# Performance work log

Measured on AMD Instinct MI355X. Metric: run time of the kernel, lower is better.

## Reference

```python
import jax, jax.numpy as jnp
import numpy as np

B, T, C, H, E, MIN_E = 4, 2048, 1024, 128, 16, 2
IS_CAUSAL = False


def setup_inputs() -> dict:
    key = jax.random.key(0)
    ks = jax.random.split(key, 6)
    lim_qkv = float(np.sqrt(6.0 / (C + H)))
    inp = {
        "hidden_states": jax.random.normal(ks[0], (B, T, C), jnp.float32),
        "sim_matrix": jax.random.normal(ks[1], (C, E), jnp.float32),
        "gates": jnp.zeros((E,), jnp.float32),
        "q_proj": jax.random.uniform(ks[2], (E, C, H), jnp.float32, -lim_qkv, lim_qkv),
        "k_proj": jax.random.uniform(ks[3], (E, C, H), jnp.float32, -lim_qkv, lim_qkv),
        "v_proj": jax.random.uniform(ks[4], (E, C, H), jnp.float32, -lim_qkv, lim_qkv),
        "o_proj": jax.random.uniform(ks[5], (E, H, C), jnp.float32, -lim_qkv, lim_qkv),
    }
    return inp


def _forward(hidden_states, sim_matrix, gates, q_proj, k_proj, v_proj, o_proj):
    b, t, c = hidden_states.shape
    n = b * t
    x = hidden_states.reshape(n, c)

    # ---- gating (faithful to _gating_logic) ----
    xn = x / jnp.maximum(jnp.linalg.norm(x, axis=-1, keepdims=True), 1e-12)
    sn = sim_matrix / jnp.maximum(jnp.linalg.norm(sim_matrix, axis=0, keepdims=True), 1e-12)
    logits = xn @ sn - jax.nn.sigmoid(gates)          # [n, E]
    gated = jax.nn.relu(logits)
    # STE: forward = (gated > 0), backward = identity
    hard = (gated > 0).astype(gated.dtype)
    mask = gated + jax.lax.stop_gradient(hard - gated)
    inactive = (jnp.sum(hard, axis=1) == 0)
    # fallback: top-MIN_E logits for tokens with no active expert
    _, fb_idx = jax.lax.top_k(logits, MIN_E)
    fb = jnp.zeros((n, logits.shape[1]), gated.dtype).at[
        jnp.arange(n)[:, None], fb_idx].set(1.0)
    put = jax.lax.stop_gradient(inactive[:, None].astype(gated.dtype) * fb)
    mask = mask * (1.0 - put) + put                   # index_put semantics
    masked = jnp.where(mask > 0, gated, -jnp.inf)
    w = jax.nn.softmax(masked, axis=-1)               # routing weights [n, E]

    # ---- MoE dispatch/combine (dense-equivalent: w is exactly 0 where mask==0) ----
    def moe_proj(p):  # p: [E, C, H] -> [n, H]
        y = jnp.einsum('nc,ech->neh', x, p)
        return jnp.einsum('ne,neh->nh', w, y)

    q = moe_proj(q_proj).reshape(b, t, -1)
    k = moe_proj(k_proj).reshape(b, t, -1)
    v = moe_proj(v_proj).reshape(b, t, -1)

    # single-head SDPA, default scale 1/sqrt(head_dim)
    h = q.shape[-1]
    scores = jnp.einsum('bth,bsh->bts', q, k) / jnp.sqrt(jnp.asarray(h, q.dtype))
    if IS_CAUSAL and t > 1:
        causal = jnp.tril(jnp.ones((t, t), bool))
        scores = jnp.where(causal[None], scores, -jnp.inf)
    attn = jax.nn.softmax(scores, axis=-1)
    o = jnp.einsum('bts,bsh->bth', attn, v).reshape(n, h)

    # output MoE combine
    z = jnp.einsum('ne,nh->enh', w, o)                # [E, n, H]
    out = jnp.einsum('enh,ehc->nc', z, o_proj)
    return out.reshape(b, t, c)


def reference(hidden_states, sim_matrix, gates, q_proj, k_proj, v_proj, o_proj):
    return _forward(hidden_states, sim_matrix, gates, q_proj, k_proj, v_proj, o_proj)
```

## Files before the change

### kernel.cpp

```cpp
#include <hip/hip_runtime.h>
#include <hip/hip_bf16.h>
#include <math.h>

#define NBATCH 4
#define NT     2048
#define NC     1024
#define NH     128
#define NE     16
#define NTOK   (NBATCH * NT)
#define CAP    18432
#define NTILE_MAX 304

typedef __bf16 bf16x8 __attribute__((ext_vector_type(8)));
typedef __bf16 bf16x4 __attribute__((ext_vector_type(4)));
typedef float  f32x4  __attribute__((ext_vector_type(4)));

__device__ __forceinline__ __bf16 f2bf(float f) { return (__bf16)f; }

#define BARRIER() __builtin_amdgcn_s_barrier()
#define SFENCE()  __builtin_amdgcn_sched_barrier(0)
#define VMWAIT(n) asm volatile("s_waitcnt vmcnt(" #n ")" ::: "memory")
#define LGKMWAIT0() asm volatile("s_waitcnt lgkmcnt(0)" ::: "memory")

__device__ __forceinline__ void gl_lds16(const void* g, void* l) {
  __builtin_amdgcn_global_load_lds((const __attribute__((address_space(1))) void*)g,
                                   (__attribute__((address_space(3))) void*)l, 16, 0, 0);
}

__device__ __forceinline__ const __bf16* swz_src(const __bf16* row0, size_t stride,
                                                 int tid, int i) {
  int lin = (tid + 256 * i) * 16;
  int r = lin >> 7, cb = lin & 127;
  return row0 + (size_t)r * stride + ((cb ^ ((r & 7) << 4)) >> 1);
}

__global__ void k_prep(const float* __restrict__ sim, const float* __restrict__ gates,
                       double* __restrict__ snorm, double* __restrict__ sig) {
  int tid = threadIdx.x;
  int e = tid & 15, chunk = tid >> 4;
  double a = 0.0;
#pragma unroll 4
  for (int j = 0; j < 64; j++) {
    double v = (double)sim[(chunk * 64 + j) * NE + e];
    a += v * v;
  }
  __shared__ double red[16][17];
  red[chunk][e] = a;
  __syncthreads();
  if (tid < 16) {
    double s = 0.0;
    for (int k = 0; k < 16; k++) s += red[k][tid];
    snorm[tid] = fmax(sqrt(s), 1e-12);
    sig[tid] = 1.0 / (1.0 + exp(-(double)gates[tid]));
  }
}

__global__ __launch_bounds__(256, 1) void k_gating3(const float* __restrict__ x,
                                                    const float* __restrict__ sim,
                                                    const double* __restrict__ snorm,
                                                    const double* __restrict__ sig,
                                                    float* __restrict__ w_all,
                                                    int* __restrict__ counts,
                                                    __bf16* __restrict__ xbf) {
  __shared__ union {
    struct {
      float xs_[32][66];
      float ss_[16][66];
    } s;
    double red[8][32][4][17];
  } u;
  __shared__ float w_lds[32][16];
  __shared__ int cnt_lds[16];
  int tid = threadIdx.x;
  if (tid < 16) cnt_lds[tid] = 0;
  int cg = tid & 31, tkg = tid >> 5;
  int tok0 = blockIdx.x * 32;

  double acc[4][17];
#pragma unroll
  for (int t = 0; t < 4; t++)
#pragma unroll
    for (int i = 0; i < 17; i++) acc[t][i] = 0.0;

  int xr0 = tid >> 4, xc4 = (tid & 15) * 4;
  int sr = tid >> 2, se4 = (tid & 3) * 4;

  float4 xa, xb, sv;
  auto ldchunk = [&](int c0) {
    xa = *(const float4*)(x + (size_t)(tok0 + xr0) * NC + c0 + xc4);
    xb = *(const float4*)(x + (size_t)(tok0 + xr0 + 16) * NC + c0 + xc4);
    sv = *(const float4*)(sim + (size_t)(c0 + sr) * NE + se4);
  };
  auto stchunk = [&]() {
    *(float4*)&u.s.xs_[xr0][xc4] = xa;
    *(float4*)&u.s.xs_[xr0 + 16][xc4] = xb;
    u.s.ss_[se4 + 0][sr] = sv.x;
    u.s.ss_[se4 + 1][sr] = sv.y;
    u.s.ss_[se4 + 2][sr] = sv.z;
    u.s.ss_[se4 + 3][sr] = sv.w;
  };
  auto stxbf = [&](int c0) {
    bf16x4 a, b;
    a[0]=f2bf(xa.x); a[1]=f2bf(xa.y); a[2]=f2bf(xa.z); a[3]=f2bf(xa.w);
    b[0]=f2bf(xb.x); b[1]=f2bf(xb.y); b[2]=f2bf(xb.z); b[3]=f2bf(xb.w);
    *(bf16x4*)(xbf + (size_t)(tok0 + xr0) * NC + c0 + xc4) = a;
    *(bf16x4*)(xbf + (size_t)(tok0 + xr0 + 16) * NC + c0 + xc4) = b;
  };

  ldchunk(0);
  for (int ch = 0; ch < 16; ch++) {
    stchunk();
    stxbf(ch * 64);
    __syncthreads();
    if (ch < 15) ldchunk((ch + 1) * 64);
    double xd[4][2];
#pragma unroll
    for (int t = 0; t < 4; t++) {
      float2 xv = *(const float2*)&u.s.xs_[tkg * 4 + t][cg * 2];
      xd[t][0] = (double)xv.x;
      xd[t][1] = (double)xv.y;
      acc[t][16] += xd[t][0] * xd[t][0] + xd[t][1] * xd[t][1];
    }
#pragma unroll
    for (int e = 0; e < 16; e++) {
      float2 sv2 = *(const float2*)&u.s.ss_[e][cg * 2];
      double s0 = (double)sv2.x, s1 = (double)sv2.y;
#pragma unroll
      for (int t = 0; t < 4; t++)
        acc[t][e] += xd[t][0] * s0 + xd[t][1] * s1;
    }
    __syncthreads();
  }

#pragma unroll
  for (int t = 0; t < 4; t++)
#pragma unroll
    for (int i = 0; i < 17; i++)
      u.red[tkg][cg][t][i] = acc[t][i];
  __syncthreads();

  if (tid < 32) {
    double dots[17];
    for (int i = 0; i < 17; i++) {
      double s = 0.0;
      for (int c = 0; c < 32; c++) s += u.red[tid >> 2][c][tid & 3][i];
      dots[i] = s;
    }
    double xn = fmax(sqrt(dots[16]), 1e-12);
    double logits[NE];
    unsigned act = 0;
    int cnt = 0;
    for (int ee = 0; ee < NE; ee++) {
      logits[ee] = dots[ee] / (xn * snorm[ee]) - sig[ee];
      if (logits[ee] > 0.0) { act |= 1u << ee; cnt++; }
    }
    if (cnt == 0) {
      int i1 = 0; double b1 = logits[0];
      for (int ee = 1; ee < NE; ee++) if (logits[ee] > b1) { b1 = logits[ee]; i1 = ee; }
      int i2 = -1; double b2 = -1e300;
      for (int ee = 0; ee < NE; ee++) if (ee != i1 && logits[ee] > b2) { b2 = logits[ee]; i2 = ee; }
      act = (1u << i1) | (1u << i2);
    }
    double m = -1e300;
    for (int ee = 0; ee < NE; ee++) if ((act >> ee) & 1) m = fmax(m, fmax(logits[ee], 0.0));
    double s = 0.0, wvv[NE];
    for (int ee = 0; ee < NE; ee++) {
      if ((act >> ee) & 1) { wvv[ee] = exp(fmax(logits[ee], 0.0) - m); s += wvv[ee]; }
      else wvv[ee] = 0.0;
    }
    for (int ee = 0; ee < NE; ee++) {
      if ((act >> ee) & 1) {
        w_lds[tid][ee] = (float)(wvv[ee] / s);
        atomicAdd(&cnt_lds[ee], 1);
      } else w_lds[tid][ee] = 0.0f;
    }
  }
  __syncthreads();
  *(float2*)&w_all[(size_t)(tok0 + (tid >> 3)) * NE + (tid & 7) * 2] =
      *(const float2*)&w_lds[tid >> 3][(tid & 7) * 2];
  if (tid < 16 && cnt_lds[tid] > 0) atomicAdd(&counts[tid], cnt_lds[tid]);
}

__global__ void k_transpose_all(const float* __restrict__ qp, const float* __restrict__ kp,
                                const float* __restrict__ vp, const float* __restrict__ op,
                                __bf16* __restrict__ pqt, __bf16* __restrict__ pkt,
                                __bf16* __restrict__ pvt, __bf16* __restrict__ pot) {
  __shared__ float tile[32][33];
  int z = blockIdx.y;
  const float* in;
  __bf16* out;
  int R, Cd, g, r0, c0;
  if (z < 48) {
    int which = z >> 4; g = z & 15; R = 1024; Cd = 128;
    in = which == 0 ? qp : (which == 1 ? kp : vp);
    out = which == 0 ? pqt : (which == 1 ? pkt : pvt);
    r0 = (blockIdx.x >> 2) * 32; c0 = (blockIdx.x & 3) * 32;
  } else {
    g = z - 48; R = 128; Cd = 1024;
    in = op; out = pot;
    r0 = (blockIdx.x & 3) * 32; c0 = (blockIdx.x >> 2) * 32;
  }
  int tx = threadIdx.x & 31, ty0 = threadIdx.x >> 5;
  const float* src = in + (size_t)g * R * Cd;
  __bf16* dst = out + (size_t)g * R * Cd;
#pragma unroll
  for (int ty = ty0; ty < 32; ty += 8)
    tile[ty][tx] = src[(size_t)(r0 + ty) * Cd + (c0 + tx)];
  __syncthreads();
#pragma unroll
  for (int ty = ty0; ty < 32; ty += 8)
    dst[(size_t)(c0 + ty) * R + (r0 + tx)] = f2bf(tile[tx][ty]);
}

__global__ void k_transpose_bf(const __bf16* __restrict__ in, __bf16* __restrict__ out,
                               int R, int Cd) {
  __shared__ __bf16 tile[32][34];
  int g = blockIdx.z;
  int r0 = blockIdx.x * 32, c0 = blockIdx.y * 32;
  int tx = threadIdx.x & 31, ty0 = threadIdx.x >> 5;
  const __bf16* src = in + (size_t)g * R * Cd;
  __bf16* dst = out + (size_t)g * R * Cd;
#pragma unroll
  for (int ty = ty0; ty < 32; ty += 8)
    tile[ty][tx] = src[(size_t)(r0 + ty) * Cd + (c0 + tx)];
  __syncthreads();
#pragma unroll
  for (int ty = ty0; ty < 32; ty += 8)
    dst[(size_t)(c0 + ty) * R + (r0 + tx)] = tile[tx][ty];
}

__global__ void k_scan(const int* __restrict__ counts, int* __restrict__ offsets,
                       int2* __restrict__ tile_desc, int* __restrict__ n_tiles) {
  if (threadIdx.x == 0 && blockIdx.x == 0) {
    int off = 0, nt = 0;
    for (int e = 0; e < NE; e++) {
      offsets[e] = off;
      int c = counts[e];
      int tiles = (c + 63) >> 6;
      for (int t = 0; t < tiles; t++) {
        int s0 = off + t * 64;
        if (s0 < CAP && nt < NTILE_MAX) { tile_desc[nt].x = e; tile_desc[nt].y = s0; nt++; }
      }
      off += c;
    }
    offsets[NE] = off;
    *n_tiles = nt;
  }
}

__global__ void k_assign(const float* __restrict__ w_all, const int* __restrict__ offsets,
                         int* __restrict__ cursors, int* __restrict__ slot_token,
                         float* __restrict__ slot_w, int* __restrict__ tok_slots,
                         int* __restrict__ tok_cnt) {
  int n = blockIdx.x * 256 + threadIdx.x;
  if (n >= NTOK) return;
  int j = 0;
  for (int e = 0; e < NE; e++) {
    float w = w_all[(size_t)n * NE + e];
    if (w > 0.0f) {
      int p = atomicAdd(&cursors[e], 1);
      int s = offsets[e] + p;
      slot_token[s] = n;
      slot_w[s] = w;
      tok_slots[n * 16 + j] = s;
      j++;
    }
  }
  tok_cnt[n] = j;
}

__device__ __forceinline__ void mfma_block(const __bf16* As, const __bf16* Bs,
                                           int lane, int wrow, f32x4 acc[8]) {
  const char* Ab = (const char*)As;
  const char* Bb = (const char*)Bs;
  int arow = wrow + (lane & 15);
  int rb = lane & 15;
#pragma unroll
  for (int ks = 0; ks < 2; ks++) {
    int kb = ks * 64 + (lane >> 4) * 16;
    bf16x8 af = *(const bf16x8*)(Ab + arow * 128 + (kb ^ ((arow & 7) << 4)));
#pragma unroll
    for (int nt = 0; nt < 8; nt++) {
      int brow = nt * 16 + rb;
      bf16x8 bv = *(const bf16x8*)(Bb + brow * 128 + (kb ^ ((brow & 7) << 4)));
      acc[nt] = __builtin_amdgcn_mfma_f32_16x16x32_bf16(af, bv, acc[nt], 0, 0, 0);
    }
  }
}

__device__ __forceinline__ void mfma_regA(bf16x8 af0, bf16x8 af1, const __bf16* Bs,
                                          int lane, f32x4 acc[8]) {
  const char* Bb = (const char*)Bs;
  int rb = lane & 15;
#pragma unroll
  for (int ks = 0; ks < 2; ks++) {
    int kb = ks * 64 + (lane >> 4) * 16;
    bf16x8 af = ks ? af1 : af0;
#pragma unroll
    for (int nt = 0; nt < 8; nt++) {
      int brow = nt * 16 + rb;
      bf16x8 bv = *(const bf16x8*)(Bb + brow * 128 + (kb ^ ((brow & 7) << 4)));
      acc[nt] = __builtin_amdgcn_mfma_f32_16x16x32_bf16(af, bv, acc[nt], 0, 0, 0);
    }
  }
}

__global__ __launch_bounds__(256) void k_moe_qkv2(
    const __bf16* __restrict__ xbf, const int* __restrict__ slot_token,
    const __bf16* __restrict__ pq, const __bf16* __restrict__ pk, const __bf16* __restrict__ pv,
    const int* __restrict__ offsets, const int2* __restrict__ tile_desc,
    const int* __restrict__ n_tiles,
    __bf16* __restrict__ yq, __bf16* __restrict__ yk, __bf16* __restrict__ yv) {
  int id = blockIdx.x;
  int w = (id & 7) * (3 * NTILE_MAX / 8) + (id >> 3);
  int ti = w / 3, p = w % 3;
  if (ti >= *n_tiles) return;
  int2 td = tile_desc[ti];
  int e = td.x, s0 = td.y;
  int seg_end = offsets[e + 1]; if (seg_end > CAP) seg_end = CAP;
  const __bf16* Bt;
  __bf16* Yd;
  if (p == 0)      { Bt = pq; Yd = yq; }
  else if (p == 1) { Bt = pk; Yd = yk; }
  else             { Bt = pv; Yd = yv; }
  Bt += (size_t)e * NH * NC;

  __shared__ __bf16 As[2][64 * 64];
  __shared__ __bf16 Bs[2][128 * 64];
  int tid = threadIdx.x, lane = tid & 63, wid = tid >> 6, wrow = wid * 16;
  const __bf16* asrc[2];
  const __bf16* bsrc[4];
#pragma unroll
  for (int i = 0; i < 2; i++) {
    int lin = (tid + 256 * i) * 16;
    int r = lin >> 7, cb = lin & 127;
    int tok = slot_token[s0 + r] & (NTOK - 1);
    asrc[i] = xbf + (size_t)tok * NC + ((cb ^ ((r & 7) << 4)) >> 1);
  }
#pragma unroll
  for (int i = 0; i < 4; i++) bsrc[i] = swz_src(Bt, NC, tid, i);
  auto stage = [&](int buf, int k0) {
#pragma unroll
    for (int i = 0; i < 2; i++)
      gl_lds16(asrc[i] + k0, (char*)As[buf] + wid * 1024 + i * 4096);
#pragma unroll
    for (int i = 0; i < 4; i++)
      gl_lds16(bsrc[i] + k0, (char*)Bs[buf] + wid * 1024 + i * 4096);
  };

  f32x4 acc[8];
#pragma unroll
  for (int i = 0; i < 8; i++) { f32x4 z = {0.f, 0.f, 0.f, 0.f}; acc[i] = z; }

  stage(0, 0);
  stage(1, 64);
  VMWAIT(6); BARRIER(); SFENCE();
  int cur = 0;
  for (int t = 0; t <= 13; t++) {
    __builtin_amdgcn_s_setprio(1);
    mfma_block(As[cur], Bs[cur], lane, wrow, acc);
    __builtin_amdgcn_s_setprio(0);
    SFENCE();
    BARRIER();
    stage(cur, (t + 2) * 64);
    VMWAIT(6); BARRIER(); SFENCE();
    cur ^= 1;
  }
  __builtin_amdgcn_s_setprio(1);
  mfma_block(As[cur], Bs[cur], lane, wrow, acc);
  __builtin_amdgcn_s_setprio(0);
  SFENCE();
  VMWAIT(0); BARRIER(); SFENCE();
  __builtin_amdgcn_s_setprio(1);
  mfma_block(As[cur ^ 1], Bs[cur ^ 1], lane, wrow, acc);
  __builtin_amdgcn_s_setprio(0);

  int col = lane & 15, quad = lane >> 4;
#pragma unroll
  for (int r = 0; r < 4; r++) {
    int s = s0 + wrow + quad * 4 + r;
    if (s < seg_end) {
#pragma unroll
      for (int nt = 0; nt < 8; nt++)
        Yd[(size_t)s * NH + nt * 16 + col] = f2bf(acc[nt][r]);
    }
  }
}

__global__ __launch_bounds__(256) void k_combine_qkv(
    const __bf16* __restrict__ yq, const __bf16* __restrict__ yk, const __bf16* __restrict__ yv,
    const int* __restrict__ tok_slots, const int* __restrict__ tok_cnt,
    const float* __restrict__ slot_w,
    __bf16* __restrict__ qb, __bf16* __restrict__ kb, __bf16* __restrict__ vb) {
  int token = blockIdx.x * 2 + (threadIdx.x >> 7);
  int h = threadIdx.x & 127;
  const __bf16* Y;
  __bf16* D;
  if (blockIdx.y == 0)      { Y = yq; D = qb; }
  else if (blockIdx.y == 1) { Y = yk; D = kb; }
  else                      { Y = yv; D = vb; }
  int cnt = tok_cnt[token];
  float acc = 0.f;
  for (int j = 0; j < cnt; j++) {
    int s = tok_slots[token * 16 + j];
    if (s < CAP) acc += slot_w[s] * (float)Y[(size_t)s * NH + h];
  }
  D[(size_t)token * NH + h] = f2bf(acc);
}

__global__ __launch_bounds__(256) void k_flash(const __bf16* __restrict__ q,
                                               const __bf16* __restrict__ k,
                                               const __bf16* __restrict__ vt,
                                               float* __restrict__ opart,
                                               float2* __restrict__ ml) {
  int id = blockIdx.x;
  int w = (id & 7) * 64 + (id >> 3);
  int b = w >> 7;
  int rem = w & 127;
  int spl = rem >> 5;
  int t0 = (rem & 31) * 64;
  const __bf16* qb = q + (size_t)b * NT * NH;
  const __bf16* kb = k + (size_t)b * NT * NH;
  const __bf16* vtb = vt + (size_t)b * NH * NT;

  __shared__ __bf16 Ks[2][128 * 64];
  __shared__ __bf16 Vs[2][128 * 64];
  __shared__ __bf16 Ps[2][64 * 64];
  int tid = threadIdx.x, lane = tid & 63, wid = tid >> 6, wrow = wid * 16;
  int colq = lane & 15, quad = lane >> 4;

  bf16x8 qf[4];
  {
    const __bf16* qr = qb + (size_t)(t0 + wrow + colq) * NH + quad * 8;
#pragma unroll
    for (int kk = 0; kk < 4; kk++) qf[kk] = *(const bf16x8*)(qr + kk * 32);
  }
  asm volatile("" :: "v"(qf[0]), "v"(qf[1]), "v"(qf[2]), "v"(qf[3]));
  SFENCE();

  auto stage_K = [&](int s0) {
#pragma unroll
    for (int c = 0; c < 2; c++)
#pragma unroll
      for (int i = 0; i < 4; i++)
        gl_lds16(swz_src(kb + (size_t)s0 * NH + c * 64, NH, tid, i),
                 (char*)Ks[c] + wid * 1024 + i * 4096);
  };
  auto stage_V = [&](int s0) {
#pragma unroll
    for (int c = 0; c < 2; c++)
#pragma unroll
      for (int i = 0; i < 4; i++)
        gl_lds16(swz_src(vtb + s0 + c * 64, NT, tid, i),
                 (char*)Vs[c] + wid * 1024 + i * 4096);
  };

  f32x4 oacc[8];
#pragma unroll
  for (int i = 0; i < 8; i++) { f32x4 z = {0.f, 0.f, 0.f, 0.f}; oacc[i] = z; }
  float mr[4], lr[4];
#pragma unroll
  for (int r = 0; r < 4; r++) { mr[r] = -1e30f; lr[r] = 0.f; }

  const int sbase = spl * 512;
  stage_K(sbase);
  stage_V(sbase);
  VMWAIT(8); BARRIER(); SFENCE();

  const float scale = 0.08838834764831843f;

  for (int t = 0; t < 4; t++) {
    f32x4 sacc[8];
#pragma unroll
    for (int i = 0; i < 8; i++) { f32x4 z = {0.f, 0.f, 0.f, 0.f}; sacc[i] = z; }
    __builtin_amdgcn_s_setprio(1);
    mfma_regA(qf[0], qf[1], Ks[0], lane, sacc);
    mfma_regA(qf[2], qf[3], Ks[1], lane, sacc);
    __builtin_amdgcn_s_setprio(0);
    SFENCE();
    BARRIER();
    if (t < 3) stage_K(sbase + (t + 1) * 128);

    float tm[4];
#pragma unroll
    for (int r = 0; r < 4; r++) {
      float v = sacc[0][r];
#pragma unroll
      for (int nt = 1; nt < 8; nt++) v = fmaxf(v, sacc[nt][r]);
      tm[r] = v * scale;
    }
#pragma unroll
    for (int off = 1; off < 16; off <<= 1)
#pragma unroll
      for (int r = 0; r < 4; r++) tm[r] = fmaxf(tm[r], __shfl_xor(tm[r], off));
    float alpha[4], rs[4];
#pragma unroll
    for (int r = 0; r < 4; r++) {
      float mn = fmaxf(mr[r], tm[r]);
      alpha[r] = expf(mr[r] - mn);
      mr[r] = mn;
      rs[r] = 0.f;
    }
#pragma unroll
    for (int nt = 0; nt < 8; nt++) {
      char* pc = (char*)Ps[nt >> 2];
      int colb = ((nt & 3) * 16 + colq) * 2;
#pragma unroll
      for (int r = 0; r < 4; r++) {
        int row = wrow + quad * 4 + r;
        float p = expf(sacc[nt][r] * scale - mr[r]);
        rs[r] += p;
        *(__bf16*)(pc + row * 128 + (colb ^ ((row & 7) << 4))) = f2bf(p);
      }
    }
#pragma unroll
    for (int off = 1; off < 16; off <<= 1)
#pragma unroll
      for (int r = 0; r < 4; r++) rs[r] += __shfl_xor(rs[r], off);
#pragma unroll
    for (int r = 0; r < 4; r++) lr[r] = alpha[r] * lr[r] + rs[r];
#pragma unroll
    for (int nt = 0; nt < 8; nt++)
#pragma unroll
      for (int r = 0; r < 4; r++) oacc[nt][r] *= alpha[r];

    LGKMWAIT0();
    if (t < 3) { VMWAIT(8); } else { VMWAIT(0); }
    BARRIER(); SFENCE();

    __builtin_amdgcn_s_setprio(1);
    mfma_block(Ps[0], Vs[0], lane, wrow, oacc);
    mfma_block(Ps[1], Vs[1], lane, wrow, oacc);
    __builtin_amdgcn_s_setprio(0);
    SFENCE();
    BARRIER();
    if (t < 3) {
      stage_V(sbase + (t + 1) * 128);
      VMWAIT(8); BARRIER(); SFENCE();
    }
  }

  size_t base = (size_t)(b * 4 + spl) * NT + t0;
#pragma unroll
  for (int r = 0; r < 4; r++) {
    size_t row = base + wrow + quad * 4 + r;
#pragma unroll
    for (int nt = 0; nt < 8; nt++)
      opart[row * NH + nt * 16 + colq] = oacc[nt][r];
  }
  if (colq == 0) {
#pragma unroll
    for (int r = 0; r < 4; r++) {
      float2 v; v.x = mr[r]; v.y = lr[r];
      ml[base + wrow + quad * 4 + r] = v;
    }
  }
}

__global__ __launch_bounds__(256) void k_gather_o(const float* __restrict__ opart,
                                                  const float2* __restrict__ ml,
                                                  const int* __restrict__ slot_token,
                                                  const int* __restrict__ offsets,
                                                  __bf16* __restrict__ og) {
  int slot = blockIdx.x * 2 + (threadIdx.x >> 7);
  int h = threadIdx.x & 127;
  int total = offsets[NE]; if (total > CAP) total = CAP;
  if (slot >= total) return;
  int n = slot_token[slot];
  int b = n >> 11, trow = n & 2047;
  size_t rb = (size_t)b * 4 * NT + trow;
  float2 m0 = ml[rb], m1 = ml[rb + NT], m2 = ml[rb + 2 * NT], m3 = ml[rb + 3 * NT];
  float M = fmaxf(fmaxf(m0.x, m1.x), fmaxf(m2.x, m3.x));
  float e0 = expf(m0.x - M), e1 = expf(m1.x - M), e2 = expf(m2.x - M), e3 = expf(m3.x - M);
  float den = m0.y * e0 + m1.y * e1 + m2.y * e2 + m3.y * e3;
  float num = opart[rb * NH + h] * e0 + opart[(rb + NT) * NH + h] * e1 +
              opart[(rb + 2 * NT) * NH + h] * e2 + opart[(rb + 3 * NT) * NH + h] * e3;
  og[(size_t)slot * NH + h] = f2bf(num / den);
}

__global__ __launch_bounds__(256) void k_out2(
    const __bf16* __restrict__ og, const __bf16* __restrict__ pot,
    const int* __restrict__ offsets, const int2* __restrict__ tile_desc,
    const int* __restrict__ n_tiles, __bf16* __restrict__ zy) {
  int id = blockIdx.x;
  int w = (id & 7) * NTILE_MAX + (id >> 3);
  int ti = w >> 3, p = w & 7;
  if (ti >= *n_tiles) return;
  int2 td = tile_desc[ti];
  int e = td.x, s0 = td.y;
  int seg_end = offsets[e + 1]; if (seg_end > CAP) seg_end = CAP;
  int nc0 = p * 128;
  const __bf16* Bt = pot + (size_t)e * NC * NH;

  __shared__ __bf16 As[2][64 * 64];
  __shared__ __bf16 Bs[2][128 * 64];
  int tid = threadIdx.x, lane = tid & 63, wid = tid >> 6, wrow = wid * 16;
  const __bf16* asrc[2];
  const __bf16* bsrc[4];
#pragma unroll
  for (int i = 0; i < 2; i++) asrc[i] = swz_src(og + (size_t)s0 * NH, NH, tid, i);
#pragma unroll
  for (int i = 0; i < 4; i++) bsrc[i] = swz_src(Bt + (size_t)nc0 * NH, NH, tid, i);
  auto stage = [&](int buf, int k0) {
#pragma unroll
    for (int i = 0; i < 2; i++)
      gl_lds16(asrc[i] + k0, (char*)As[buf] + wid * 1024 + i * 4096);
#pragma unroll
    for (int i = 0; i < 4; i++)
      gl_lds16(bsrc[i] + k0, (char*)Bs[buf] + wid * 1024 + i * 4096);
  };
  f32x4 acc[8];
#pragma unroll
  for (int i = 0; i < 8; i++) { f32x4 z = {0.f, 0.f, 0.f, 0.f}; acc[i] = z; }

  stage(0, 0);
  stage(1, 64);
  VMWAIT(6); BARRIER(); SFENCE();
  __builtin_amdgcn_s_setprio(1);
  mfma_block(As[0], Bs[0], lane, wrow, acc);
  __builtin_amdgcn_s_setprio(0);
  SFENCE();
  VMWAIT(0); BARRIER(); SFENCE();
  __builtin_amdgcn_s_setprio(1);
  mfma_block(As[1], Bs[1], lane, wrow, acc);
  __builtin_amdgcn_s_setprio(0);

  int col = lane & 15, quad = lane >> 4;
#pragma unroll
  for (int r = 0; r < 4; r++) {
    int s = s0 + wrow + quad * 4 + r;
    if (s < seg_end) {
#pragma unroll
      for (int nt = 0; nt < 8; nt++)
        zy[(size_t)s * NC + nc0 + nt * 16 + col] = f2bf(acc[nt][r]);
    }
  }
}

__global__ __launch_bounds__(256) void k_combine_out(
    const __bf16* __restrict__ zy, const int* __restrict__ tok_slots,
    const int* __restrict__ tok_cnt, const float* __restrict__ slot_w,
    float* __restrict__ out) {
  int token = blockIdx.x;
  int c = threadIdx.x * 4;
  int cnt = tok_cnt[token];
  float a0 = 0.f, a1 = 0.f, a2 = 0.f, a3 = 0.f;
  for (int j = 0; j < cnt; j++) {
    int s = tok_slots[token * 16 + j];
    if (s < CAP) {
      float w = slot_w[s];
      bf16x4 z = *(const bf16x4*)&zy[(size_t)s * NC + c];
      a0 += w * (float)z[0];
      a1 += w * (float)z[1];
      a2 += w * (float)z[2];
      a3 += w * (float)z[3];
    }
  }
  float4 o = {a0, a1, a2, a3};
  *(float4*)&out[(size_t)token * NC + c] = o;
}

extern "C" void kernel_launch(void* const* d_in, const int* in_sizes, int n_in,
                              void* d_out, int out_size, void* d_ws, size_t ws_size,
                              hipStream_t stream) {
  const float* hs    = (const float*)d_in[0];
  const float* sim   = (const float*)d_in[1];
  const float* gates = (const float*)d_in[2];
  const float* qp    = (const float*)d_in[3];
  const float* kp    = (const float*)d_in[4];
  const float* vp    = (const float*)d_in[5];
  const float* op    = (const float*)d_in[6];
  float* out = (float*)d_out;
  char* ws = (char*)d_ws;

  const size_t M = 1048576;
  __bf16* PQT = (__bf16*)(ws + 0 * M);
  __bf16* PKT = (__bf16*)(ws + 4 * M);
  __bf16* PVT = (__bf16*)(ws + 8 * M);
  __bf16* POT = (__bf16*)(ws + 12 * M);
  __bf16* Qb  = (__bf16*)(ws + 16 * M);
  __bf16* Kb  = (__bf16*)(ws + 18 * M);
  __bf16* Vb  = (__bf16*)(ws + 20 * M);
  __bf16* VT  = (__bf16*)(ws + 22 * M);
  float*  WALL = (float*)(ws + 28 * M);
  int*    STOK = (int*)(ws + 28 * M + 524288);
  float*  SW   = (float*)(ws + 28 * M + 1048576);
  int*    TSL  = (int*)(ws + 28 * M + 1572864);
  int*    TCN  = (int*)(ws + 28 * M + 2097152);
  double* SNORM = (double*)(ws + 28 * M + 2129920);
  double* SIG   = SNORM + 16;
  int* CNT = (int*)(ws + 28 * M + 2130432);
  int* OFF = CNT + 16;
  int* CUR = CNT + 40;
  int* NTL = CNT + 60;
  int2* DESC = (int2*)(ws + 28 * M + 2131456);
  __bf16* XBF = (__bf16*)(ws + 32 * M);
  __bf16* YQ = (__bf16*)(ws + 72 * M);
  __bf16* YK = (__bf16*)(ws + 77 * M);
  __bf16* YV = (__bf16*)(ws + 82 * M);
  float*  OP2 = (float*)(ws + 32 * M);
  float2* MLB = (float2*)(ws + 50 * M);
  __bf16* OG = (__bf16*)(ws + 52 * M);
  __bf16* ZY = (__bf16*)(ws + 60 * M);

  hipMemsetAsync(CNT, 0, 512, stream);

  k_prep<<<1, 256, 0, stream>>>(sim, gates, SNORM, SIG);
  k_transpose_all<<<dim3(128, 64), 256, 0, stream>>>(qp, kp, vp, op, PQT, PKT, PVT, POT);
  k_gating3<<<NTOK / 32, 256, 0, stream>>>(hs, sim, SNORM, SIG, WALL, CNT, XBF);
  k_scan<<<1, 64, 0, stream>>>(CNT, OFF, DESC, NTL);
  k_assign<<<NTOK / 256, 256, 0, stream>>>(WALL, OFF, CUR, STOK, SW, TSL, TCN);
  k_moe_qkv2<<<3 * NTILE_MAX, 256, 0, stream>>>(XBF, STOK, PQT, PKT, PVT, OFF, DESC, NTL, YQ, YK, YV);
  k_combine_qkv<<<dim3(NTOK / 2, 3), 256, 0, stream>>>(YQ, YK, YV, TSL, TCN, SW, Qb, Kb, Vb);
  k_transpose_bf<<<dim3(64, 4, 4), 256, 0, stream>>>(Vb, VT, 2048, 128);
  k_flash<<<512, 256, 0, stream>>>(Qb, Kb, VT, OP2, MLB);
  k_gather_o<<<CAP / 2, 256, 0, stream>>>(OP2, MLB, STOK, OFF, OG);
  k_out2<<<8 * NTILE_MAX, 256, 0, stream>>>(OG, POT, OFF, DESC, NTL, ZY);
  k_combine_out<<<NTOK, 256, 0, stream>>>(ZY, TSL, TCN, SW, out);
}
```

Measured before the change: 305.8 us.

## Double MoE GEMM tile rows to 128 and fold k_prep into transpose kernel

The expert-grouped GEMMs for the QKV projections and the output projection now use 128-row slot tiles instead of 64. Each wave computes two 16-row MFMA fragments that share the same B operand loads, and the tile count and grid sizes are halved to match. This raises reuse of each staged weight tile and cuts the number of blocks, at the cost of more padding waste in partially filled expert segments, larger LDS use, and more accumulator registers. Separately, the sim-norm and sigmoid prep kernel is merged into the transpose launch as an extra grid row, saving one kernel launch.

```diff
diff --git a/kernel.cpp b/kernel.cpp
--- a/kernel.cpp
+++ b/kernel.cpp
@@ -9,7 +9,7 @@
 #define NE     16
 #define NTOK   (NBATCH * NT)
 #define CAP    18432
-#define NTILE_MAX 304
+#define NT2_MAX 152
 
 typedef __bf16 bf16x8 __attribute__((ext_vector_type(8)));
 typedef __bf16 bf16x4 __attribute__((ext_vector_type(4)));
@@ -34,25 +34,58 @@
   return row0 + (size_t)r * stride + ((cb ^ ((r & 7) << 4)) >> 1);
 }
 
-__global__ void k_prep(const float* __restrict__ sim, const float* __restrict__ gates,
-                       double* __restrict__ snorm, double* __restrict__ sig) {
+__global__ void k_transpose_all(const float* __restrict__ qp, const float* __restrict__ kp,
+                                const float* __restrict__ vp, const float* __restrict__ op,
+                                __bf16* __restrict__ pqt, __bf16* __restrict__ pkt,
+                                __bf16* __restrict__ pvt, __bf16* __restrict__ pot,
+                                const float* __restrict__ sim, const float* __restrict__ gates,
+                                double* __restrict__ snorm, double* __restrict__ sig) {
+  __shared__ float tile[32][33];
+  __shared__ double red[16][17];
+  int z = blockIdx.y;
   int tid = threadIdx.x;
-  int e = tid & 15, chunk = tid >> 4;
-  double a = 0.0;
+  if (z == 64) {
+    if (blockIdx.x != 0) return;
+    int e = tid & 15, chunk = tid >> 4;
+    double a = 0.0;
 #pragma unroll 4
-  for (int j = 0; j < 64; j++) {
-    double v = (double)sim[(chunk * 64 + j) * NE + e];
-    a += v * v;
-  }
-  __shared__ double red[16][17];
-  red[chunk][e] = a;
+    for (int j = 0; j < 64; j++) {
+      double v = (double)sim[(chunk * 64 + j) * NE + e];
+      a += v * v;
+    }
+    red[chunk][e] = a;
+    __syncthreads();
+    if (tid < 16) {
+      double s = 0.0;
+      for (int k = 0; k < 16; k++) s += red[k][tid];
+      snorm[tid] = fmax(sqrt(s), 1e-12);
+      sig[tid] = 1.0 / (1.0 + exp(-(double)gates[tid]));
+    }
+    return;
+  }
+  const float* in;
+  __bf16* out;
+  int R, Cd, g, r0, c0;
+  if (z < 48) {
+    int which = z >> 4; g = z & 15; R = 1024; Cd = 128;
+    in = which == 0 ? qp : (which == 1 ? kp : vp);
+    out = which == 0 ? pqt : (which == 1 ? pkt : pvt);
+    r0 = (blockIdx.x >> 2) * 32; c0 = (blockIdx.x & 3) * 32;
+  } else {
+    g = z - 48; R = 128; Cd = 1024;
+    in = op; out = pot;
+    r0 = (blockIdx.x & 3) * 32; c0 = (blockIdx.x >> 2) * 32;
+  }
+  int tx = tid & 31, ty0 = tid >> 5;
+  const float* src = in + (size_t)g * R * Cd;
+  __bf16* dst = out + (size_t)g * R * Cd;
+#pragma unroll
+  for (int ty = ty0; ty < 32; ty += 8)
+    tile[ty][tx] = src[(size_t)(r0 + ty) * Cd + (c0 + tx)];
   __syncthreads();
-  if (tid < 16) {
-    double s = 0.0;
-    for (int k = 0; k < 16; k++) s += red[k][tid];
-    snorm[tid] = fmax(sqrt(s), 1e-12);
-    sig[tid] = 1.0 / (1.0 + exp(-(double)gates[tid]));
-  }
+#pragma unroll
+  for (int ty = ty0; ty < 32; ty += 8)
+    dst[(size_t)(c0 + ty) * R + (r0 + tx)] = f2bf(tile[tx][ty]);
 }
 
 __global__ __launch_bounds__(256, 1) void k_gating3(const float* __restrict__ x,
@@ -181,37 +214,6 @@
   if (tid < 16 && cnt_lds[tid] > 0) atomicAdd(&counts[tid], cnt_lds[tid]);
 }
 
-__global__ void k_transpose_all(const float* __restrict__ qp, const float* __restrict__ kp,
-                                const float* __restrict__ vp, const float* __restrict__ op,
-                                __bf16* __restrict__ pqt, __bf16* __restrict__ pkt,
-                                __bf16* __restrict__ pvt, __bf16* __restrict__ pot) {
-  __shared__ float tile[32][33];
-  int z = blockIdx.y;
-  const float* in;
-  __bf16* out;
-  int R, Cd, g, r0, c0;
-  if (z < 48) {
-    int which = z >> 4; g = z & 15; R = 1024; Cd = 128;
-    in = which == 0 ? qp : (which == 1 ? kp : vp);
-    out = which == 0 ? pqt : (which == 1 ? pkt : pvt);
-    r0 = (blockIdx.x >> 2) * 32; c0 = (blockIdx.x & 3) * 32;
-  } else {
-    g = z - 48; R = 128; Cd = 1024;
-    in = op; out = pot;
-    r0 = (blockIdx.x & 3) * 32; c0 = (blockIdx.x >> 2) * 32;
-  }
-  int tx = threadIdx.x & 31, ty0 = threadIdx.x >> 5;
-  const float* src = in + (size_t)g * R * Cd;
-  __bf16* dst = out + (size_t)g * R * Cd;
-#pragma unroll
-  for (int ty = ty0; ty < 32; ty += 8)
-    tile[ty][tx] = src[(size_t)(r0 + ty) * Cd + (c0 + tx)];
-  __syncthreads();
-#pragma unroll
-  for (int ty = ty0; ty < 32; ty += 8)
-    dst[(size_t)(c0 + ty) * R + (r0 + tx)] = f2bf(tile[tx][ty]);
-}
-
 __global__ void k_transpose_bf(const __bf16* __restrict__ in, __bf16* __restrict__ out,
                                int R, int Cd) {
   __shared__ __bf16 tile[32][34];
@@ -236,10 +238,10 @@
     for (int e = 0; e < NE; e++) {
       offsets[e] = off;
       int c = counts[e];
-      int tiles = (c + 63) >> 6;
+      int tiles = (c + 127) >> 7;
       for (int t = 0; t < tiles; t++) {
-        int s0 = off + t * 64;
-        if (s0 < CAP && nt < NTILE_MAX) { tile_desc[nt].x = e; tile_desc[nt].y = s0; nt++; }
+        int s0 = off + t * 128;
+        if (s0 < CAP && nt < NT2_MAX) { tile_desc[nt].x = e; tile_desc[nt].y = s0; nt++; }
       }
       off += c;
     }
@@ -288,6 +290,28 @@
   }
 }
 
+__device__ __forceinline__ void mfma_block128(const __bf16* As, const __bf16* Bs,
+                                              int lane, int wrow2, f32x4 acc[2][8]) {
+  const char* Ab = (const char*)As;
+  const char* Bb = (const char*)Bs;
+  int rb = lane & 15;
+#pragma unroll
+  for (int ks = 0; ks < 2; ks++) {
+    int kb = ks * 64 + (lane >> 4) * 16;
+    int ar = wrow2 + rb;
+    int sw = kb ^ ((ar & 7) << 4);
+    bf16x8 af0 = *(const bf16x8*)(Ab + ar * 128 + sw);
+    bf16x8 af1 = *(const bf16x8*)(Ab + (ar + 16) * 128 + sw);
+#pragma unroll
+    for (int nt = 0; nt < 8; nt++) {
+      int brow = nt * 16 + rb;
+      bf16x8 bv = *(const bf16x8*)(Bb + brow * 128 + (kb ^ ((brow & 7) << 4)));
+      acc[0][nt] = __builtin_amdgcn_mfma_f32_16x16x32_bf16(af0, bv, acc[0][nt], 0, 0, 0);
+      acc[1][nt] = __builtin_amdgcn_mfma_f32_16x16x32_bf16(af1, bv, acc[1][nt], 0, 0, 0);
+    }
+  }
+}
+
 __device__ __forceinline__ void mfma_regA(bf16x8 af0, bf16x8 af1, const __bf16* Bs,
                                           int lane, f32x4 acc[8]) {
   const char* Bb = (const char*)Bs;
@@ -312,7 +336,7 @@
     const int* __restrict__ n_tiles,
     __bf16* __restrict__ yq, __bf16* __restrict__ yk, __bf16* __restrict__ yv) {
   int id = blockIdx.x;
-  int w = (id & 7) * (3 * NTILE_MAX / 8) + (id >> 3);
+  int w = (id & 7) * (3 * NT2_MAX / 8) + (id >> 3);
   int ti = w / 3, p = w % 3;
   if (ti >= *n_tiles) return;
   int2 td = tile_desc[ti];
@@ -325,13 +349,13 @@
   else             { Bt = pv; Yd = yv; }
   Bt += (size_t)e * NH * NC;
 
-  __shared__ __bf16 As[2][64 * 64];
+  __shared__ __bf16 As[2][128 * 64];
   __shared__ __bf16 Bs[2][128 * 64];
-  int tid = threadIdx.x, lane = tid & 63, wid = tid >> 6, wrow = wid * 16;
-  const __bf16* asrc[2];
+  int tid = threadIdx.x, lane = tid & 63, wid = tid >> 6, wrow2 = wid * 32;
+  const __bf16* asrc[4];
   const __bf16* bsrc[4];
 #pragma unroll
-  for (int i = 0; i < 2; i++) {
+  for (int i = 0; i < 4; i++) {
     int lin = (tid + 256 * i) * 16;
     int r = lin >> 7, cb = lin & 127;
     int tok = slot_token[s0 + r] & (NTOK - 1);
@@ -341,50 +365,54 @@
   for (int i = 0; i < 4; i++) bsrc[i] = swz_src(Bt, NC, tid, i);
   auto stage = [&](int buf, int k0) {
 #pragma unroll
-    for (int i = 0; i < 2; i++)
-      gl_lds16(asrc[i] + k0, (char*)As[buf] + wid * 1024 + i * 4096);
-#pragma unroll
     for (int i = 0; i < 4; i++)
-      gl_lds16(bsrc[i] + k0, (char*)Bs[buf] + wid * 1024 + i * 4096);
+      gl_lds16(asrc[i] + k0, (char*)As[buf] + tid * 16 + i * 4096);
+#pragma unroll
+    for (int i = 0; i < 4; i++)
+      gl_lds16(bsrc[i] + k0, (char*)Bs[buf] + tid * 16 + i * 4096);
   };
 
-  f32x4 acc[8];
-#pragma unroll
-  for (int i = 0; i < 8; i++) { f32x4 z = {0.f, 0.f, 0.f, 0.f}; acc[i] = z; }
+  f32x4 acc[2][8];
+#pragma unroll
+  for (int rf = 0; rf < 2; rf++)
+#pragma unroll
+    for (int i = 0; i < 8; i++) { f32x4 z = {0.f, 0.f, 0.f, 0.f}; acc[rf][i] = z; }
 
   stage(0, 0);
   stage(1, 64);
-  VMWAIT(6); BARRIER(); SFENCE();
+  VMWAIT(8); BARRIER(); SFENCE();
   int cur = 0;
   for (int t = 0; t <= 13; t++) {
     __builtin_amdgcn_s_setprio(1);
-    mfma_block(As[cur], Bs[cur], lane, wrow, acc);
+    mfma_block128(As[cur], Bs[cur], lane, wrow2, acc);
     __builtin_amdgcn_s_setprio(0);
     SFENCE();
     BARRIER();
     stage(cur, (t + 2) * 64);
-    VMWAIT(6); BARRIER(); SFENCE();
+    VMWAIT(8); BARRIER(); SFENCE();
     cur ^= 1;
   }
   __builtin_amdgcn_s_setprio(1);
-  mfma_block(As[cur], Bs[cur], lane, wrow, acc);
+  mfma_block128(As[cur], Bs[cur], lane, wrow2, acc);
   __builtin_amdgcn_s_setprio(0);
   SFENCE();
   VMWAIT(0); BARRIER(); SFENCE();
   __builtin_amdgcn_s_setprio(1);
-  mfma_block(As[cur ^ 1], Bs[cur ^ 1], lane, wrow, acc);
+  mfma_block128(As[cur ^ 1], Bs[cur ^ 1], lane, wrow2, acc);
   __builtin_amdgcn_s_setprio(0);
 
   int col = lane & 15, quad = lane >> 4;
 #pragma unroll
-  for (int r = 0; r < 4; r++) {
-    int s = s0 + wrow + quad * 4 + r;
-    if (s < seg_end) {
-#pragma unroll
-      for (int nt = 0; nt < 8; nt++)
-        Yd[(size_t)s * NH + nt * 16 + col] = f2bf(acc[nt][r]);
-    }
-  }
+  for (int rf = 0; rf < 2; rf++)
+#pragma unroll
+    for (int r = 0; r < 4; r++) {
+      int s = s0 + wrow2 + rf * 16 + quad * 4 + r;
+      if (s < seg_end) {
+#pragma unroll
+        for (int nt = 0; nt < 8; nt++)
+          Yd[(size_t)s * NH + nt * 16 + col] = f2bf(acc[rf][nt][r]);
+      }
+    }
 }
 
 __global__ __launch_bounds__(256) void k_combine_qkv(
@@ -583,7 +611,7 @@
     const int* __restrict__ offsets, const int2* __restrict__ tile_desc,
     const int* __restrict__ n_tiles, __bf16* __restrict__ zy) {
   int id = blockIdx.x;
-  int w = (id & 7) * NTILE_MAX + (id >> 3);
+  int w = (id & 7) * NT2_MAX + (id >> 3);
   int ti = w >> 3, p = w & 7;
   if (ti >= *n_tiles) return;
   int2 td = tile_desc[ti];
@@ -592,49 +620,53 @@
   int nc0 = p * 128;
   const __bf16* Bt = pot + (size_t)e * NC * NH;
 
-  __shared__ __bf16 As[2][64 * 64];
+  __shared__ __bf16 As[2][128 * 64];
   __shared__ __bf16 Bs[2][128 * 64];
-  int tid = threadIdx.x, lane = tid & 63, wid = tid >> 6, wrow = wid * 16;
-  const __bf16* asrc[2];
+  int tid = threadIdx.x, lane = tid & 63, wid = tid >> 6, wrow2 = wid * 32;
+  const __bf16* asrc[4];
   const __bf16* bsrc[4];
 #pragma unroll
-  for (int i = 0; i < 2; i++) asrc[i] = swz_src(og + (size_t)s0 * NH, NH, tid, i);
+  for (int i = 0; i < 4; i++) asrc[i] = swz_src(og + (size_t)s0 * NH, NH, tid, i);
 #pragma unroll
   for (int i = 0; i < 4; i++) bsrc[i] = swz_src(Bt + (size_t)nc0 * NH, NH, tid, i);
   auto stage = [&](int buf, int k0) {
 #pragma unroll
-    for (int i = 0; i < 2; i++)
-      gl_lds16(asrc[i] + k0, (char*)As[buf] + wid * 1024 + i * 4096);
-#pragma unroll
     for (int i = 0; i < 4; i++)
-      gl_lds16(bsrc[i] + k0, (char*)Bs[buf] + wid * 1024 + i * 4096);
+      gl_lds16(asrc[i] + k0, (char*)As[buf] + tid * 16 + i * 4096);
+#pragma unroll
+    for (int i = 0; i < 4; i++)
+      gl_lds16(bsrc[i] + k0, (char*)Bs[buf] + tid * 16 + i * 4096);
   };
-  f32x4 acc[8];
-#pragma unroll
-  for (int i = 0; i < 8; i++) { f32x4 z = {0.f, 0.f, 0.f, 0.f}; acc[i] = z; }
+  f32x4 acc[2][8];
+#pragma unroll
+  for (int rf = 0; rf < 2; rf++)
+#pragma unroll
+    for (int i = 0; i < 8; i++) { f32x4 z = {0.f, 0.f, 0.f, 0.f}; acc[rf][i] = z; }
 
   stage(0, 0);
   stage(1, 64);
-  VMWAIT(6); BARRIER(); SFENCE();
+  VMWAIT(8); BARRIER(); SFENCE();
   __builtin_amdgcn_s_setprio(1);
-  mfma_block(As[0], Bs[0], lane, wrow, acc);
+  mfma_block128(As[0], Bs[0], lane, wrow2, acc);
   __builtin_amdgcn_s_setprio(0);
   SFENCE();
   VMWAIT(0); BARRIER(); SFENCE();
   __builtin_amdgcn_s_setprio(1);
-  mfma_block(As[1], Bs[1], lane, wrow, acc);
+  mfma_block128(As[1], Bs[1], lane, wrow2, acc);
   __builtin_amdgcn_s_setprio(0);
 
   int col = lane & 15, quad = lane >> 4;
 #pragma unroll
-  for (int r = 0; r < 4; r++) {
-    int s = s0 + wrow + quad * 4 + r;
-    if (s < seg_end) {
-#pragma unroll
-      for (int nt = 0; nt < 8; nt++)
-        zy[(size_t)s * NC + nc0 + nt * 16 + col] = f2bf(acc[nt][r]);
-    }
-  }
+  for (int rf = 0; rf < 2; rf++)
+#pragma unroll
+    for (int r = 0; r < 4; r++) {
+      int s = s0 + wrow2 + rf * 16 + quad * 4 + r;
+      if (s < seg_end) {
+#pragma unroll
+        for (int nt = 0; nt < 8; nt++)
+          zy[(size_t)s * NC + nc0 + nt * 16 + col] = f2bf(acc[rf][nt][r]);
+      }
+    }
 }
 
 __global__ __launch_bounds__(256) void k_combine_out(
@@ -705,16 +737,16 @@
 
   hipMemsetAsync(CNT, 0, 512, stream);
 
-  k_prep<<<1, 256, 0, stream>>>(sim, gates, SNORM, SIG);
-  k_transpose_all<<<dim3(128, 64), 256, 0, stream>>>(qp, kp, vp, op, PQT, PKT, PVT, POT);
+  k_transpose_all<<<dim3(128, 65), 256, 0, stream>>>(qp, kp, vp, op, PQT, PKT, PVT, POT,
+                                                     sim, gates, SNORM, SIG);
   k_gating3<<<NTOK / 32, 256, 0, stream>>>(hs, sim, SNORM, SIG, WALL, CNT, XBF);
   k_scan<<<1, 64, 0, stream>>>(CNT, OFF, DESC, NTL);
   k_assign<<<NTOK / 256, 256, 0, stream>>>(WALL, OFF, CUR, STOK, SW, TSL, TCN);
-  k_moe_qkv2<<<3 * NTILE_MAX, 256, 0, stream>>>(XBF, STOK, PQT, PKT, PVT, OFF, DESC, NTL, YQ, YK, YV);
+  k_moe_qkv2<<<3 * NT2_MAX, 256, 0, stream>>>(XBF, STOK, PQT, PKT, PVT, OFF, DESC, NTL, YQ, YK, YV);
   k_combine_qkv<<<dim3(NTOK / 2, 3), 256, 0, stream>>>(YQ, YK, YV, TSL, TCN, SW, Qb, Kb, Vb);
   k_transpose_bf<<<dim3(64, 4, 4), 256, 0, stream>>>(Vb, VT, 2048, 128);
   k_flash<<<512, 256, 0, stream>>>(Qb, Kb, VT, OP2, MLB);
   k_gather_o<<<CAP / 2, 256, 0, stream>>>(OP2, MLB, STOK, OFF, OG);
-  k_out2<<<8 * NTILE_MAX, 256, 0, stream>>>(OG, POT, OFF, DESC, NTL, ZY);
+  k_out2<<<8 * NT2_MAX, 256, 0, stream>>>(OG, POT, OFF, DESC, NTL, ZY);
   k_combine_out<<<NTOK, 256, 0, stream>>>(ZY, TSL, TCN, SW, out);
 }
```

After: 287.8 us. 1.06x faster.
